# Kernel tuning notes

Hardware: AMD Instinct MI355X
Metric: run time of the kernel (lower is better)

## Reference

```python
import jax, jax.numpy as jnp
import numpy as np

N_CONTEXT = 8
N_ANS = 8


def _g_mlp(x, Wg1, bg1, Wg2, bg2, Wg3, bg3):
    # 3-layer relation MLP G, applied per object pair
    h = jax.nn.relu(x @ Wg1 + bg1)
    h = jax.nn.relu(h @ Wg2 + bg2)
    return jax.nn.relu(h @ Wg3 + bg3)


def setup_inputs() -> dict:
    key = jax.random.key(0)
    ks = jax.random.split(key, 12)
    B, P, C, H, W = 512, 16, 1, 80, 80
    D = 512                      # embedding_dim
    T = 2 * (D + 9)              # object_tuple_size = 1042
    s = jnp.float32(0.02)
    f32 = jnp.float32
    return {
        "x": jax.random.normal(ks[0], (B, P, C, H, W), f32),
        "W_emb": jax.random.normal(ks[1], (C * H * W, D), f32) * s,
        "b_emb": jnp.zeros((D,), f32),
        "Wg1": jax.random.normal(ks[2], (T, T), f32) * s,
        "bg1": jnp.zeros((T,), f32),
        "Wg2": jax.random.normal(ks[3], (T, T), f32) * s,
        "bg2": jnp.zeros((T,), f32),
        "Wg3": jax.random.normal(ks[4], (T, T), f32) * s,
        "bg3": jnp.zeros((T,), f32),
        "Wf1": jax.random.normal(ks[5], (T, T), f32) * s,
        "bf1": jnp.zeros((T,), f32),
        "Wf2": jax.random.normal(ks[6], (T, 1), f32) * s,
        "bf2": jnp.zeros((1,), f32),
        "labels_idx": jax.random.randint(ks[7], (B,), 0, N_ANS),
    }


def reference(x, W_emb, b_emb, Wg1, bg1, Wg2, bg2, Wg3, bg3,
              Wf1, bf1, Wf2, bf2, labels_idx):
    B = x.shape[0]
    D = W_emb.shape[1]
    # frozen embedding (torch.no_grad) -> stop_gradient
    emb = jax.lax.stop_gradient(
        x.reshape(B * (N_CONTEXT + N_ANS), -1) @ W_emb + b_emb
    ).reshape(B, N_CONTEXT + N_ANS, D)

    # TagPanelEmbeddings: context panels -> one-hot 0..7, answers -> one-hot 8 (9 dims)
    eye9 = jnp.eye(9, dtype=emb.dtype)
    tags = jnp.concatenate([eye9[:N_CONTEXT],
                            jnp.tile(eye9[8:9], (N_ANS, 1))], axis=0)  # (16, 9)
    tagged = jnp.concatenate(
        [emb, jnp.broadcast_to(tags, (B, N_CONTEXT + N_ANS, 9))], axis=-1)  # (B,16,D+9)

    ctx = tagged[:, :N_CONTEXT]   # (B,8,d)
    cho = tagged[:, N_CONTEXT:]   # (B,8,d)
    d = ctx.shape[-1]

    # all 8x8 ordered context pairs: pair[i,j] = concat(obj_j, obj_i)
    ctx_pairs = jnp.concatenate([
        jnp.broadcast_to(ctx[:, None, :, :], (B, 8, 8, d)),
        jnp.broadcast_to(ctx[:, :, None, :], (B, 8, 8, d)),
    ], axis=-1).reshape(B, 64, 2 * d)
    ctx_g = _g_mlp(ctx_pairs, Wg1, bg1, Wg2, bg2, Wg3, bg3).sum(axis=1)  # (B,T)

    # context-choice pairs, vectorized over all 8 answers:
    # pair[a,k] = concat(context_k, choice_a)  -> (B, N_ANS, 8, 2d)
    cc_pairs = jnp.concatenate([
        jnp.broadcast_to(ctx[:, None, :, :], (B, N_ANS, 8, d)),
        jnp.broadcast_to(cho[:, :, None, :], (B, N_ANS, 8, d)),
    ], axis=-1)
    cc_g = _g_mlp(cc_pairs, Wg1, bg1, Wg2, bg2, Wg3, bg3).sum(axis=2)  # (B,N_ANS,T)

    relations = ctx_g[:, None, :] + cc_g  # (B,N_ANS,T); norm = Identity

    # F readout: 2-layer MLP to scalar per answer
    h = jax.nn.relu(relations @ Wf1 + bf1)
    f_out = (h @ Wf2 + bf2)[..., 0]  # (B, N_ANS)

    labels = jax.nn.one_hot(labels_idx, N_ANS, dtype=f_out.dtype)
    # stable BCE-with-logits, mean over all elements
    loss = jnp.mean(jnp.maximum(f_out, 0) - f_out * labels
                    + jnp.log1p(jnp.exp(-jnp.abs(f_out))))
    preds = jnp.argmax(f_out, axis=1)
    acc = jnp.mean((preds == labels_idx).astype(f_out.dtype))
    return loss, acc
```

## Files before the change

kernel.cpp:

```cpp
#include <hip/hip_runtime.h>
#include <hip/hip_bf16.h>
#include <math.h>


typedef __bf16 bf16;
typedef __bf16 v8bf __attribute__((ext_vector_type(8)));
typedef float  v4f  __attribute__((ext_vector_type(4)));
typedef unsigned long long u64;

#define GAS(p) ((const __attribute__((address_space(1))) void*)(p))
#define LAS(p) ((__attribute__((address_space(3))) void*)(p))

__global__ __launch_bounds__(256) void gemm_bf16(
    const bf16* __restrict__ A, int lda,
    const bf16* __restrict__ Bt, int ldb,
    bf16* __restrict__ C, int ldc,
    int Mt, int Nt,
    int Nreal, int Nstore, int K,
    const float* __restrict__ bias,
    const float* __restrict__ tagW, int tag_ld,
    int relu, int mode)
{
    __shared__ bf16 As[128 * 32];
    __shared__ bf16 Bs[128 * 32];
    __shared__ bf16 Epi[64 * 132];

    const int L    = blockIdx.x;
    const int xcd  = L & 7;
    const int idx  = L >> 3;
    const int mlee = idx / Nt;
    const int n    = idx - mlee * Nt;
    const int m    = xcd * (Mt >> 3) + mlee;
    const int row0 = m * 128;
    const int col0 = n * 128;

    const int tid  = threadIdx.x;
    const int wv   = tid >> 6;
    const int lane = tid & 63;
    const int quad = lane >> 4;
    const int l15  = lane & 15;
    const int wm0  = (wv >> 1) * 64;
    const int wn0  = (wv & 1) * 64;

    v4f acc[4][4] = {};

    const int srow  = wv * 32 + (lane >> 2);
    const int skoff = (lane & 3) * 8;
    const bf16* ga = A  + (size_t)(row0 + srow) * lda + skoff;
    const bf16* gb = Bt + (size_t)(col0 + srow) * ldb + skoff;
    bf16* laA = &As[(wv * 32) * 32];
    bf16* laB = &Bs[(wv * 32) * 32];

    for (int k0 = 0; k0 < K; k0 += 32) {
        __builtin_amdgcn_global_load_lds(GAS(ga),                    LAS(laA),           16, 0, 0);
        __builtin_amdgcn_global_load_lds(GAS(ga + (size_t)16 * lda), LAS(laA + 16 * 32), 16, 0, 0);
        __builtin_amdgcn_global_load_lds(GAS(gb),                    LAS(laB),           16, 0, 0);
        __builtin_amdgcn_global_load_lds(GAS(gb + (size_t)16 * ldb), LAS(laB + 16 * 32), 16, 0, 0);
        ga += 32; gb += 32;
        __syncthreads();

        v8bf af[4], bf[4];
        #pragma unroll
        for (int i = 0; i < 4; ++i)
            af[i] = *(const v8bf*)&As[(wm0 + i * 16 + l15) * 32 + quad * 8];
        #pragma unroll
        for (int j = 0; j < 4; ++j)
            bf[j] = *(const v8bf*)&Bs[(wn0 + j * 16 + l15) * 32 + quad * 8];
        #pragma unroll
        for (int i = 0; i < 4; ++i)
            #pragma unroll
            for (int j = 0; j < 4; ++j)
                acc[i][j] = __builtin_amdgcn_mfma_f32_16x16x32_bf16(af[i], bf[j], acc[i][j], 0, 0, 0);
        __syncthreads();
    }

    float bcol[4];
    #pragma unroll
    for (int j = 0; j < 4; ++j) {
        int col = col0 + wn0 + j * 16 + l15;
        bcol[j] = (col < Nreal && bias) ? bias[col] : 0.f;
    }

    float s_ctx = 0.f;

    #pragma unroll
    for (int pass = 0; pass < 2; ++pass) {
        if (wm0 == pass * 64) {
            #pragma unroll
            for (int i = 0; i < 4; ++i) {
                #pragma unroll
                for (int j = 0; j < 4; ++j) {
                    #pragma unroll
                    for (int r = 0; r < 4; ++r) {
                        int lrow = i * 16 + quad * 4 + r;
                        int lcol = wn0 + j * 16 + l15;
                        int col  = col0 + lcol;
                        float v = 0.f;
                        if (col < Nreal) {
                            v = acc[i][j][r] + bcol[j];
                            if (tagW) {
                                int row = row0 + pass * 64 + lrow;
                                int tp = row & 15; if (tp > 8) tp = 8;
                                v += tagW[(size_t)tp * tag_ld + col];
                            }
                            if (relu) v = fmaxf(v, 0.f);
                        }
                        Epi[lrow * 132 + lcol] = (bf16)v;
                    }
                }
            }
        }
        __syncthreads();

        if (mode == 0) {
            int lrow = tid >> 2;
            int cg   = (tid & 3) * 32;
            int grow = row0 + pass * 64 + lrow;
            #pragma unroll
            for (int k = 0; k < 4; ++k) {
                int c = cg + k * 8;
                int gcol = col0 + c;
                if (gcol < Nstore) {
                    u64 q0 = *(const u64*)&Epi[lrow * 132 + c];
                    u64 q1 = *(const u64*)&Epi[lrow * 132 + c + 4];
                    uint4 st;
                    st.x = (unsigned)q0; st.y = (unsigned)(q0 >> 32);
                    st.z = (unsigned)q1; st.w = (unsigned)(q1 >> 32);
                    *(uint4*)&C[(size_t)grow * ldc + gcol] = st;
                }
            }
        } else {
            if (tid < 128) {
                int col = tid;
                if (pass == 0) {
                    float s = 0.f;
                    for (int r = 0; r < 64; ++r) s += (float)Epi[r * 132 + col];
                    s_ctx = s;
                } else {
                    float sA[8] = {};
                    for (int r = 0; r < 64; ++r) sA[r >> 3] += (float)Epi[r * 132 + col];
                    int gcol = col0 + col;
                    if (gcol < Nstore) {
                        #pragma unroll
                        for (int a = 0; a < 8; ++a)
                            C[(size_t)(m * 8 + a) * ldc + gcol] = (bf16)(s_ctx + sA[a]);
                    }
                }
            }
        }
        __syncthreads();
    }
}

__global__ void transpose_cast(const float* __restrict__ W, int ldw,
                               int krows, int ncols,
                               bf16* __restrict__ Bt, int ldb,
                               int nalloc, int kalloc)
{
    __shared__ float t[32][33];
    int kb = blockIdx.x * 32;
    int nb = blockIdx.y * 32;
    int tx = threadIdx.x, ty = threadIdx.y;
    #pragma unroll
    for (int i = 0; i < 4; ++i) {
        int k = kb + ty + i * 8, n = nb + tx;
        t[ty + i * 8][tx] = (k < krows && n < ncols) ? W[(size_t)k * ldw + n] : 0.f;
    }
    __syncthreads();
    #pragma unroll
    for (int i = 0; i < 4; ++i) {
        int n = nb + ty + i * 8, k = kb + tx;
        if (n < nalloc && k < kalloc)
            Bt[(size_t)n * ldb + k] = (bf16)t[tx][ty + i * 8];
    }
}

__global__ void cast_bf16_vec(const float* __restrict__ in, bf16* __restrict__ out, size_t n4)
{
    size_t i = blockIdx.x * (size_t)blockDim.x + threadIdx.x;
    if (i >= n4) return;
    float4 v = ((const float4*)in)[i];
    union { bf16 h[4]; u64 q; } o;
    o.h[0] = (bf16)v.x; o.h[1] = (bf16)v.y; o.h[2] = (bf16)v.z; o.h[3] = (bf16)v.w;
    *(u64*)&out[i * 4] = o.q;
}

__global__ void pair_build(const bf16* __restrict__ U, const bf16* __restrict__ V,
                           bf16* __restrict__ H1, int ldp)
{
    int r = blockIdx.x;
    int p = r & 127, bb = r >> 7;
    const bf16* ur = U + (size_t)(bb * 16 + (p & 7)) * ldp;
    const bf16* vr = V + (size_t)(bb * 16 + (p >> 3)) * ldp;
    bf16* hr = H1 + (size_t)r * ldp;
    int nch = ldp >> 3;
    for (int c8 = threadIdx.x; c8 < nch; c8 += blockDim.x) {
        v8bf u = *(const v8bf*)&ur[c8 * 8];
        v8bf v = *(const v8bf*)&vr[c8 * 8];
        v8bf o;
        #pragma unroll
        for (int i = 0; i < 8; ++i)
            o[i] = (bf16)fmaxf((float)u[i] + (float)v[i], 0.f);
        *(v8bf*)&hr[c8 * 8] = o;
    }
}

__global__ void fout_kernel(const bf16* __restrict__ h, const float* __restrict__ Wf2,
                            const float* __restrict__ bf2, float* __restrict__ fout,
                            int rows, int T, int ldp)
{
    int wid  = (int)((blockIdx.x * (size_t)blockDim.x + threadIdx.x) >> 6);
    int lane = threadIdx.x & 63;
    if (wid >= rows) return;
    const bf16* hr = h + (size_t)wid * ldp;
    float s = 0.f;
    for (int c = lane; c < T; c += 64) s += (float)hr[c] * Wf2[c];
    #pragma unroll
    for (int off = 32; off > 0; off >>= 1) s += __shfl_down(s, off, 64);
    if (lane == 0) fout[wid] = s + bf2[0];
}

__global__ void loss_kernel(const float* __restrict__ fout, const int* __restrict__ labels,
                            float* __restrict__ out)
{
    __shared__ float sl[512];
    __shared__ float sc[512];
    int b = threadIdx.x;
    const float* f = fout + (size_t)b * 8;
    int lab = labels[b];
    float rl = 0.f;
    int best = 0;
    float bv = f[0];
    #pragma unroll
    for (int a = 0; a < 8; ++a) {
        float v = f[a];
        rl += fmaxf(v, 0.f) - v * ((a == lab) ? 1.f : 0.f) + log1pf(expf(-fabsf(v)));
        if (v > bv) { bv = v; best = a; }
    }
    sl[b] = rl;
    sc[b] = (best == lab) ? 1.f : 0.f;
    __syncthreads();
    for (int s = 256; s > 0; s >>= 1) {
        if (b < s) { sl[b] += sl[b + s]; sc[b] += sc[b + s]; }
        __syncthreads();
    }
    if (b == 0) { out[0] = sl[0] / 4096.f; out[1] = sc[0] / 512.f; }
}

extern "C" void kernel_launch(void* const* d_in, const int* in_sizes, int n_in,
                              void* d_out, int out_size, void* d_ws, size_t ws_size,
                              hipStream_t stream)
{
    (void)in_sizes; (void)n_in; (void)out_size;
    const float* x      = (const float*)d_in[0];
    const float* W_emb  = (const float*)d_in[1];
    const float* b_emb  = (const float*)d_in[2];
    const float* Wg1    = (const float*)d_in[3];
    const float* bg1    = (const float*)d_in[4];
    const float* Wg2    = (const float*)d_in[5];
    const float* bg2    = (const float*)d_in[6];
    const float* Wg3    = (const float*)d_in[7];
    const float* bg3    = (const float*)d_in[8];
    const float* Wf1    = (const float*)d_in[9];
    const float* bf1    = (const float*)d_in[10];
    const float* Wf2    = (const float*)d_in[11];
    const float* bf2    = (const float*)d_in[12];
    const int*   labels = (const int*)d_in[13];

    const int B = 512, S = 16, E = 6400, D = 512, T = 1042;
    const int TP = 1056;
    const int NA = 1152;

    auto alignup = [](size_t v) { return (v + 255) & ~(size_t)255; };

    size_t fixed = alignup((size_t)B * 8 * 4)
                 + alignup((size_t)D * E * 2)
                 + 2 * alignup((size_t)NA * D * 2)
                 + 3 * alignup((size_t)NA * TP * 2);

    int Bc = 512;
    for (;;) {
        size_t need = fixed
            + alignup((size_t)Bc * S * E * 2)
            + alignup((size_t)Bc * S * D * 2)
            + 2 * alignup((size_t)Bc * S * TP * 2)
            + 2 * alignup((size_t)Bc * 128 * TP * 2)
            + alignup((size_t)Bc * 8 * TP * 2)
            + alignup((size_t)Bc * 8 * TP * 2);
        if (need <= ws_size || Bc == 16) break;
        Bc >>= 1;
    }

    char* p = (char*)d_ws;
    auto take = [&](size_t bytes) -> void* {
        char* r = p; p += (bytes + 255) & ~(size_t)255; return r;
    };
    float* fout  = (float*)take((size_t)B * 8 * 4);
    bf16* W_embT = (bf16*)take((size_t)D * E * 2);
    bf16* W1aT   = (bf16*)take((size_t)NA * D * 2);
    bf16* W1bT   = (bf16*)take((size_t)NA * D * 2);
    bf16* Wg2T   = (bf16*)take((size_t)NA * TP * 2);
    bf16* Wg3T   = (bf16*)take((size_t)NA * TP * 2);
    bf16* Wf1T   = (bf16*)take((size_t)NA * TP * 2);
    bf16* xb     = (bf16*)take((size_t)Bc * S * E * 2);
    bf16* embB   = (bf16*)take((size_t)Bc * S * D * 2);
    bf16* Ubuf   = (bf16*)take((size_t)Bc * S * TP * 2);
    bf16* Vbuf   = (bf16*)take((size_t)Bc * S * TP * 2);
    bf16* H1     = (bf16*)take((size_t)Bc * 128 * TP * 2);
    bf16* H2     = (bf16*)take((size_t)Bc * 128 * TP * 2);
    bf16* REL    = (bf16*)take((size_t)Bc * 8 * TP * 2);
    bf16* HF     = (bf16*)take((size_t)Bc * 8 * TP * 2);

    dim3 tb(32, 8);
    transpose_cast<<<dim3(E / 32, D / 32), tb, 0, stream>>>(W_emb, D, E, D, W_embT, E, D, E);
    transpose_cast<<<dim3(D / 32, NA / 32), tb, 0, stream>>>(Wg1,                   T, D, T, W1aT, D, NA, D);
    transpose_cast<<<dim3(D / 32, NA / 32), tb, 0, stream>>>(Wg1 + (size_t)521 * T, T, D, T, W1bT, D, NA, D);
    transpose_cast<<<dim3(TP / 32, NA / 32), tb, 0, stream>>>(Wg2, T, T, T, Wg2T, TP, NA, TP);
    transpose_cast<<<dim3(TP / 32, NA / 32), tb, 0, stream>>>(Wg3, T, T, T, Wg3T, TP, NA, TP);
    transpose_cast<<<dim3(TP / 32, NA / 32), tb, 0, stream>>>(Wf1, T, T, T, Wf1T, TP, NA, TP);

    const int nch = B / Bc;
    for (int ch = 0; ch < nch; ++ch) {
        const int M1t = Bc * S / 128, M2t = Bc, M3t = Bc * 8 / 128;

        size_t nx4 = (size_t)Bc * S * E / 4;
        cast_bf16_vec<<<(int)((nx4 + 255) / 256), 256, 0, stream>>>(
            x + (size_t)ch * Bc * S * E, xb, nx4);

        gemm_bf16<<<M1t * (D / 128), 256, 0, stream>>>(
            xb, E, W_embT, E, embB, D, M1t, D / 128, D, D, E, b_emb, nullptr, 0, 0, 0);

        gemm_bf16<<<M1t * (NA / 128), 256, 0, stream>>>(
            embB, D, W1aT, D, Ubuf, TP, M1t, NA / 128, T, TP, D, bg1, Wg1 + (size_t)512 * T, T, 0, 0);
        gemm_bf16<<<M1t * (NA / 128), 256, 0, stream>>>(
            embB, D, W1bT, D, Vbuf, TP, M1t, NA / 128, T, TP, D, nullptr, Wg1 + (size_t)1033 * T, T, 0, 0);

        pair_build<<<Bc * 128, 128, 0, stream>>>(Ubuf, Vbuf, H1, TP);

        gemm_bf16<<<M2t * (NA / 128), 256, 0, stream>>>(
            H1, TP, Wg2T, TP, H2, TP, M2t, NA / 128, T, TP, TP, bg2, nullptr, 0, 1, 0);
        gemm_bf16<<<M2t * (NA / 128), 256, 0, stream>>>(
            H2, TP, Wg3T, TP, REL, TP, M2t, NA / 128, T, TP, TP, bg3, nullptr, 0, 1, 1);

        gemm_bf16<<<M3t * (NA / 128), 256, 0, stream>>>(
            REL, TP, Wf1T, TP, HF, TP, M3t, NA / 128, T, TP, TP, bf1, nullptr, 0, 1, 0);

        fout_kernel<<<(Bc * 8 * 64 + 255) / 256, 256, 0, stream>>>(
            HF, Wf2, bf2, fout + (size_t)ch * Bc * 8, Bc * 8, T, TP);
    }

    loss_kernel<<<1, 512, 0, stream>>>(fout, labels, (float*)d_out);
}
```

Before: 1.236 ms.

## Add 256x256-tile pipelined GEMM kernel for relation MLP layers 2 and 3

Adds a new 512-thread GEMM kernel with 256x256 output tiles, 64-deep K steps, double-buffered LDS staging with XOR-swizzled slots, interleaved load/MFMA phases separated by barriers, and raised wave priority around the MFMA blocks. It replaces the 128x128 kernel for the two large pair-MLP layers and handles the per-context/per-answer pair-sum reduction in its epilogue using cross-lane shuffles. Padding changes to TP=1088 (a multiple of 64) and NAB=1280 for the Wg2/Wg3 weights so tiles divide evenly. The goal is more operand reuse per tile and overlap of global loads with matrix math, paid for with 128KB of dynamic shared memory, higher register pressure and some wasted work on padded columns.

After: 1.049 ms. -15.2%, faster.

```diff
diff --git a/kernel.cpp b/kernel.cpp
--- a/kernel.cpp
+++ b/kernel.cpp
@@ -59,18 +59,18 @@
         ga += 32; gb += 32;
         __syncthreads();
 
-        v8bf af[4], bf[4];
+        v8bf af[4], bfq[4];
         #pragma unroll
         for (int i = 0; i < 4; ++i)
             af[i] = *(const v8bf*)&As[(wm0 + i * 16 + l15) * 32 + quad * 8];
         #pragma unroll
         for (int j = 0; j < 4; ++j)
-            bf[j] = *(const v8bf*)&Bs[(wn0 + j * 16 + l15) * 32 + quad * 8];
+            bfq[j] = *(const v8bf*)&Bs[(wn0 + j * 16 + l15) * 32 + quad * 8];
         #pragma unroll
         for (int i = 0; i < 4; ++i)
             #pragma unroll
             for (int j = 0; j < 4; ++j)
-                acc[i][j] = __builtin_amdgcn_mfma_f32_16x16x32_bf16(af[i], bf[j], acc[i][j], 0, 0, 0);
+                acc[i][j] = __builtin_amdgcn_mfma_f32_16x16x32_bf16(af[i], bfq[j], acc[i][j], 0, 0, 0);
         __syncthreads();
     }
 
@@ -152,6 +152,201 @@
     }
 }
 
+__global__ __launch_bounds__(512, 2) void gemm256(
+    const bf16* __restrict__ A, int lda,
+    const bf16* __restrict__ Bt, int ldb,
+    bf16* __restrict__ C, int ldc,
+    int Mt, int Nt, int Nreal, int Nstore, int K,
+    const float* __restrict__ bias, int relu, int mode)
+{
+    extern __shared__ char smem[];
+    (void)relu;
+
+    const int NTK = K >> 6;
+
+    const int L    = blockIdx.x;
+    const int xcd  = L & 7;
+    const int idx  = L >> 3;
+    const int mlee = idx / Nt;
+    const int n    = idx - mlee * Nt;
+    const int m    = xcd * (Mt >> 3) + mlee;
+    const int row0 = m * 256;
+    const int col0 = n * 256;
+
+    const int tid  = threadIdx.x;
+    const int wv   = tid >> 6;
+    const int lane = tid & 63;
+    const int wr   = wv >> 2;
+    const int wc   = wv & 3;
+    const int l15  = lane & 15;
+    const int quad = lane >> 4;
+    const int s7   = l15 & 7;
+    const int slot0 = ((0 + quad) ^ s7) << 4;
+    const int slot1 = ((4 + quad) ^ s7) << 4;
+
+    char* const aB0 = smem + wr * 16384;
+    char* const bB0 = smem + 65536 + (wc >> 1) * 16384 + (wc & 1) * 8192;
+
+    const int srow = tid >> 3;
+    const int gce  = ((tid ^ srow) & 7) * 8;
+    const bf16* const Ab = A  + (size_t)(row0 + srow) * lda + gce;
+    const bf16* const Bb = Bt + (size_t)(col0 + srow) * ldb + gce;
+    char* const ldsA = smem + wv * 1024;
+    char* const ldsB = smem + 65536 + wv * 1024;
+
+#define STAGE_A(kt, h, buf) { \
+    const bf16* s0_ = Ab + (size_t)((h) * 128) * lda + (kt) * 64; \
+    char* d_ = ldsA + (buf) * 32768 + (h) * 16384; \
+    __builtin_amdgcn_global_load_lds(GAS(s0_),                    LAS(d_),        16, 0, 0); \
+    __builtin_amdgcn_global_load_lds(GAS(s0_ + (size_t)64 * lda), LAS(d_ + 8192), 16, 0, 0); }
+#define STAGE_B(kt, h, buf) { \
+    const bf16* s0_ = Bb + (size_t)((h) * 128) * ldb + (kt) * 64; \
+    char* d_ = ldsB + (buf) * 32768 + (h) * 16384; \
+    __builtin_amdgcn_global_load_lds(GAS(s0_),                    LAS(d_),        16, 0, 0); \
+    __builtin_amdgcn_global_load_lds(GAS(s0_ + (size_t)64 * ldb), LAS(d_ + 8192), 16, 0, 0); }
+
+#define LDA4(buf, qmB) \
+    _Pragma("unroll") \
+    for (int i_ = 0; i_ < 4; ++i_) { \
+        afr[i_][0] = *(const v8bf*)(aB0 + (buf) * 32768 + (((qmB) + i_) * 16 + l15) * 128 + slot0); \
+        afr[i_][1] = *(const v8bf*)(aB0 + (buf) * 32768 + (((qmB) + i_) * 16 + l15) * 128 + slot1); \
+    }
+#define LDB2(buf, nfB) \
+    _Pragma("unroll") \
+    for (int j_ = 0; j_ < 2; ++j_) { \
+        bfr[j_][0] = *(const v8bf*)(bB0 + (buf) * 32768 + (((nfB) + j_) * 16 + l15) * 128 + slot0); \
+        bfr[j_][1] = *(const v8bf*)(bB0 + (buf) * 32768 + (((nfB) + j_) * 16 + l15) * 128 + slot1); \
+    }
+#define MM8(qmB, nfB) \
+    _Pragma("unroll") \
+    for (int i_ = 0; i_ < 4; ++i_) \
+        _Pragma("unroll") \
+        for (int j_ = 0; j_ < 2; ++j_) { \
+            acc[(qmB) + i_][(nfB) + j_] = __builtin_amdgcn_mfma_f32_16x16x32_bf16(afr[i_][0], bfr[j_][0], acc[(qmB) + i_][(nfB) + j_], 0, 0, 0); \
+            acc[(qmB) + i_][(nfB) + j_] = __builtin_amdgcn_mfma_f32_16x16x32_bf16(afr[i_][1], bfr[j_][1], acc[(qmB) + i_][(nfB) + j_], 0, 0, 0); \
+        }
+#define BAR()   asm volatile("s_barrier" ::: "memory")
+#define PRIO1() __builtin_amdgcn_s_setprio(1)
+#define PRIO0() __builtin_amdgcn_s_setprio(0)
+
+    v4f acc[8][4] = {};
+    v8bf afr[4][2], bfr[2][2];
+
+    STAGE_A(0, 0, 0); STAGE_A(0, 1, 0); STAGE_B(0, 0, 0); STAGE_B(0, 1, 0);
+    if (NTK > 1) {
+        STAGE_A(1, 0, 1);
+        asm volatile("s_waitcnt vmcnt(2)" ::: "memory");
+    } else {
+        asm volatile("s_waitcnt vmcnt(0)" ::: "memory");
+    }
+    BAR();
+
+    int t = 0;
+    for (; t + 1 < NTK; t += 2) {
+        LDA4(0, 0); LDB2(0, 0); STAGE_A(t + 1, 1, 1);
+        BAR(); PRIO1(); MM8(0, 0); PRIO0(); BAR();
+        LDB2(0, 2); STAGE_B(t + 1, 0, 1);
+        BAR(); PRIO1(); MM8(0, 2); PRIO0(); BAR();
+        LDA4(0, 4); LDB2(0, 0); STAGE_B(t + 1, 1, 1);
+        BAR(); PRIO1(); MM8(4, 0); PRIO0(); BAR();
+        LDB2(0, 2);
+        if (t + 2 < NTK) STAGE_A(t + 2, 0, 0);
+        BAR(); PRIO1(); MM8(4, 2); PRIO0();
+        if (t + 2 < NTK) asm volatile("s_waitcnt vmcnt(2)" ::: "memory");
+        else             asm volatile("s_waitcnt vmcnt(0)" ::: "memory");
+        BAR();
+        LDA4(1, 0); LDB2(1, 0);
+        if (t + 2 < NTK) STAGE_A(t + 2, 1, 0);
+        BAR(); PRIO1(); MM8(0, 0); PRIO0(); BAR();
+        LDB2(1, 2);
+        if (t + 2 < NTK) STAGE_B(t + 2, 0, 0);
+        BAR(); PRIO1(); MM8(0, 2); PRIO0(); BAR();
+        LDA4(1, 4); LDB2(1, 0);
+        if (t + 2 < NTK) STAGE_B(t + 2, 1, 0);
+        BAR(); PRIO1(); MM8(4, 0); PRIO0(); BAR();
+        LDB2(1, 2);
+        if (t + 3 < NTK) STAGE_A(t + 3, 0, 1);
+        BAR(); PRIO1(); MM8(4, 2); PRIO0();
+        if (t + 3 < NTK) asm volatile("s_waitcnt vmcnt(2)" ::: "memory");
+        else             asm volatile("s_waitcnt vmcnt(0)" ::: "memory");
+        BAR();
+    }
+    if (t < NTK) {
+        LDA4(0, 0); LDB2(0, 0); BAR(); PRIO1(); MM8(0, 0); PRIO0(); BAR();
+        LDB2(0, 2);             BAR(); PRIO1(); MM8(0, 2); PRIO0(); BAR();
+        LDA4(0, 4); LDB2(0, 0); BAR(); PRIO1(); MM8(4, 0); PRIO0(); BAR();
+        LDB2(0, 2);             BAR(); PRIO1(); MM8(4, 2); PRIO0();
+    }
+
+    const int crow = row0 + wr * 128 + quad * 4;
+    const int ccol = col0 + wc * 64 + l15;
+
+    if (mode == 0) {
+        #pragma unroll
+        for (int j = 0; j < 4; ++j) {
+            int col = ccol + j * 16;
+            if (col < Nstore) {
+                bool real = col < Nreal;
+                float bc = (real && bias) ? bias[col] : 0.f;
+                #pragma unroll
+                for (int i = 0; i < 8; ++i) {
+                    #pragma unroll
+                    for (int r = 0; r < 4; ++r) {
+                        float v = 0.f;
+                        if (real) v = fmaxf(acc[i][j][r] + bc, 0.f);
+                        C[(size_t)(crow + i * 16 + r) * ldc + col] = (bf16)v;
+                    }
+                }
+            }
+        }
+    } else {
+        const int bb = (row0 >> 7) + wr;
+        #pragma unroll
+        for (int j = 0; j < 4; ++j) {
+            int col = ccol + j * 16;
+            bool real = col < Nreal;
+            float bc = (real && bias) ? bias[col] : 0.f;
+            float red[9];
+            float sc = 0.f;
+            #pragma unroll
+            for (int i = 0; i < 4; ++i)
+                #pragma unroll
+                for (int r = 0; r < 4; ++r)
+                    sc += fmaxf(acc[i][j][r] + bc, 0.f);
+            red[0] = sc;
+            #pragma unroll
+            for (int a = 0; a < 8; ++a) {
+                float s = 0.f;
+                if ((quad >> 1) == (a & 1)) {
+                    const int i = 4 + (a >> 1);
+                    #pragma unroll
+                    for (int r = 0; r < 4; ++r)
+                        s += fmaxf(acc[i][j][r] + bc, 0.f);
+                }
+                red[1 + a] = s;
+            }
+            #pragma unroll
+            for (int k = 0; k < 9; ++k) {
+                red[k] += __shfl_xor(red[k], 16, 64);
+                red[k] += __shfl_xor(red[k], 32, 64);
+            }
+            if (quad == 0 && col < Nstore) {
+                #pragma unroll
+                for (int a = 0; a < 8; ++a)
+                    C[(size_t)(bb * 8 + a) * ldc + col] = (bf16)(red[0] + red[1 + a]);
+            }
+        }
+    }
+#undef STAGE_A
+#undef STAGE_B
+#undef LDA4
+#undef LDB2
+#undef MM8
+#undef BAR
+#undef PRIO1
+#undef PRIO0
+}
+
 __global__ void transpose_cast(const float* __restrict__ W, int ldw,
                                int krows, int ncols,
                                bf16* __restrict__ Bt, int ldb,
@@ -268,15 +463,24 @@
     const int*   labels = (const int*)d_in[13];
 
     const int B = 512, S = 16, E = 6400, D = 512, T = 1042;
-    const int TP = 1056;
-    const int NA = 1152;
+    const int TP  = 1088;
+    const int NA  = 1152;
+    const int NAB = 1280;
+
+    static int attr_set = 0;
+    if (!attr_set) {
+        (void)hipFuncSetAttribute((const void*)gemm256,
+                                  hipFuncAttributeMaxDynamicSharedMemorySize, 131072);
+        attr_set = 1;
+    }
 
     auto alignup = [](size_t v) { return (v + 255) & ~(size_t)255; };
 
     size_t fixed = alignup((size_t)B * 8 * 4)
                  + alignup((size_t)D * E * 2)
                  + 2 * alignup((size_t)NA * D * 2)
-                 + 3 * alignup((size_t)NA * TP * 2);
+                 + 2 * alignup((size_t)NAB * TP * 2)
+                 + alignup((size_t)NA * TP * 2);
 
     int Bc = 512;
     for (;;) {
@@ -299,8 +503,8 @@
     bf16* W_embT = (bf16*)take((size_t)D * E * 2);
     bf16* W1aT   = (bf16*)take((size_t)NA * D * 2);
     bf16* W1bT   = (bf16*)take((size_t)NA * D * 2);
-    bf16* Wg2T   = (bf16*)take((size_t)NA * TP * 2);
-    bf16* Wg3T   = (bf16*)take((size_t)NA * TP * 2);
+    bf16* Wg2T   = (bf16*)take((size_t)NAB * TP * 2);
+    bf16* Wg3T   = (bf16*)take((size_t)NAB * TP * 2);
     bf16* Wf1T   = (bf16*)take((size_t)NA * TP * 2);
     bf16* xb     = (bf16*)take((size_t)Bc * S * E * 2);
     bf16* embB   = (bf16*)take((size_t)Bc * S * D * 2);
@@ -315,13 +519,14 @@
     transpose_cast<<<dim3(E / 32, D / 32), tb, 0, stream>>>(W_emb, D, E, D, W_embT, E, D, E);
     transpose_cast<<<dim3(D / 32, NA / 32), tb, 0, stream>>>(Wg1,                   T, D, T, W1aT, D, NA, D);
     transpose_cast<<<dim3(D / 32, NA / 32), tb, 0, stream>>>(Wg1 + (size_t)521 * T, T, D, T, W1bT, D, NA, D);
-    transpose_cast<<<dim3(TP / 32, NA / 32), tb, 0, stream>>>(Wg2, T, T, T, Wg2T, TP, NA, TP);
-    transpose_cast<<<dim3(TP / 32, NA / 32), tb, 0, stream>>>(Wg3, T, T, T, Wg3T, TP, NA, TP);
+    transpose_cast<<<dim3(TP / 32, NAB / 32), tb, 0, stream>>>(Wg2, T, T, T, Wg2T, TP, NAB, TP);
+    transpose_cast<<<dim3(TP / 32, NAB / 32), tb, 0, stream>>>(Wg3, T, T, T, Wg3T, TP, NAB, TP);
     transpose_cast<<<dim3(TP / 32, NA / 32), tb, 0, stream>>>(Wf1, T, T, T, Wf1T, TP, NA, TP);
 
     const int nch = B / Bc;
     for (int ch = 0; ch < nch; ++ch) {
-        const int M1t = Bc * S / 128, M2t = Bc, M3t = Bc * 8 / 128;
+        const int M1t = Bc * S / 128, M3t = Bc * 8 / 128;
+        const int M2t6 = Bc * 128 / 256;
 
         size_t nx4 = (size_t)Bc * S * E / 4;
         cast_bf16_vec<<<(int)((nx4 + 255) / 256), 256, 0, stream>>>(
@@ -337,10 +542,10 @@
 
         pair_build<<<Bc * 128, 128, 0, stream>>>(Ubuf, Vbuf, H1, TP);
 
-        gemm_bf16<<<M2t * (NA / 128), 256, 0, stream>>>(
-            H1, TP, Wg2T, TP, H2, TP, M2t, NA / 128, T, TP, TP, bg2, nullptr, 0, 1, 0);
-        gemm_bf16<<<M2t * (NA / 128), 256, 0, stream>>>(
-            H2, TP, Wg3T, TP, REL, TP, M2t, NA / 128, T, TP, TP, bg3, nullptr, 0, 1, 1);
+        gemm256<<<M2t6 * (NAB / 256), 512, 131072, stream>>>(
+            H1, TP, Wg2T, TP, H2, TP, M2t6, NAB / 256, T, TP, TP, bg2, 1, 0);
+        gemm256<<<M2t6 * (NAB / 256), 512, 131072, stream>>>(
+            H2, TP, Wg3T, TP, REL, TP, M2t6, NAB / 256, T, TP, TP, bg3, 1, 1);
 
         gemm_bf16<<<M3t * (NA / 128), 256, 0, stream>>>(
             REL, TP, Wf1T, TP, HF, TP, M3t, NA / 128, T, TP, TP, bf1, nullptr, 0, 1, 0);
```
